# Kernel tuning notes

Measured on AMD Instinct MI355X. Metric: run time of the kernel, lower is better.

The kernel has to match this reference:

```python
import jax, jax.numpy as jnp
import numpy as np

MARGIN = 0.3
N, D = 8192, 128
NUM_CLASSES = 512


def setup_inputs() -> dict:
    key = jax.random.key(0)
    k1, k2 = jax.random.split(key)
    embeddings = jax.random.normal(k1, (N, D), dtype=jnp.float32)
    targets = jax.random.randint(k2, (N,), 0, NUM_CLASSES, dtype=jnp.int64)
    return {"embeddings": embeddings, "targets": targets}


def reference(embeddings, targets):
    x = embeddings.astype(jnp.float32)
    # pairwise squared-euclidean: ||xi||^2 + ||xj||^2 - 2 xi.xj, clamped then sqrt
    sq = jnp.sum(x * x, axis=1)  # [N]
    dist = sq[:, None] + sq[None, :] - 2.0 * (x @ x.T)
    dist = jnp.sqrt(jnp.clip(dist, 1e-12, None))  # [N, N]

    is_pos = targets[:, None] == targets[None, :]  # includes diagonal, as in torch code

    # batch-hard mining: per-row hardest positive (max) and hardest negative (min)
    dist_ap = jnp.max(jnp.where(is_pos, dist, -jnp.inf), axis=1)
    dist_an = jnp.min(jnp.where(is_pos, jnp.inf, dist), axis=1)

    # MarginRankingLoss(margin)(dist_an, dist_ap, y=1) = mean(relu(margin - (dist_an - dist_ap)))
    loss = jnp.mean(jax.nn.relu(dist_ap - dist_an + MARGIN))
    return loss
```

## Files before the change

kernel.cpp:

```cpp
#include <hip/hip_runtime.h>
#include <hip/hip_bf16.h>

#define N_ROWS 8192
#define DIM 128
#define MARGIN_F 0.3f

typedef __attribute__((ext_vector_type(8))) short short8;
typedef __attribute__((ext_vector_type(4))) float f32x4;

__global__ __launch_bounds__(256) void prep_kernel(
    const float* __restrict__ x, const int* __restrict__ tgt,
    unsigned short* __restrict__ xbA, unsigned short* __restrict__ xbB,
    float2* __restrict__ meta, int* __restrict__ apb, int* __restrict__ anb,
    unsigned long long* __restrict__ lsum, unsigned int* __restrict__ lcnt) {
  if (blockIdx.x == 0 && threadIdx.x == 0) { *lsum = 0ull; *lcnt = 0u; }
  const int w = threadIdx.x >> 6, l = threadIdx.x & 63;
  const int row = blockIdx.x * 4 + w;
  float2 v = reinterpret_cast<const float2*>(x + (size_t)row * DIM)[l];
  __hip_bfloat16 b0 = __float2bfloat16(v.x);
  __hip_bfloat16 b1 = __float2bfloat16(v.y);
  __hip_bfloat16 a0 = __float2bfloat16(-2.f * v.x);
  __hip_bfloat16 a1 = __float2bfloat16(-2.f * v.y);
  ushort2 stB, stA;
  stB.x = *reinterpret_cast<unsigned short*>(&b0);
  stB.y = *reinterpret_cast<unsigned short*>(&b1);
  stA.x = *reinterpret_cast<unsigned short*>(&a0);
  stA.y = *reinterpret_cast<unsigned short*>(&a1);
  const int c16 = row >> 4, l15r = row & 15;
  const int unit = c16 * 256 + (l >> 4) * 64 + ((l >> 2) & 3) * 16 + l15r;
  reinterpret_cast<ushort2*>(xbB)[unit * 4 + (l & 3)] = stB;
  reinterpret_cast<ushort2*>(xbA)[unit * 4 + (l & 3)] = stA;

  float s = v.x * v.x + v.y * v.y;
  #pragma unroll
  for (int off = 32; off >= 1; off >>= 1) s += __shfl_xor(s, off);
  if (l == 0) {
    float2 m;
    m.x = s;
    m.y = __int_as_float(tgt[row]);
    meta[row] = m;
    apb[row] = 0x00000000;
    anb[row] = 0x7f800000;
  }
}

__global__ __launch_bounds__(256, 4) void gram_mine_kernel(
    const unsigned short* __restrict__ xbA, const unsigned short* __restrict__ xbB,
    const float2* __restrict__ meta, int* __restrict__ apb, int* __restrict__ anb) {
  const int t = threadIdx.x;
  const int w = t >> 6, l = t & 63;
  const int l15 = l & 15, l4 = l >> 4;
  const int rb = blockIdx.x * 128 + w * 32;
  const int chunk = blockIdx.y * 256;
  const int chunkb = chunk >> 4;

  const short8* xfA = reinterpret_cast<const short8*>(xbA);
  const short8* xfB = reinterpret_cast<const short8*>(xbB);

  short8 a0[4], a1[4];
  #pragma unroll
  for (int kk = 0; kk < 4; ++kk) {
    a0[kk] = xfA[(rb >> 4) * 256 + kk * 64 + l];
    a1[kk] = xfA[((rb >> 4) + 1) * 256 + kk * 64 + l];
  }

  int t_r[8];
  #pragma unroll
  for (int rf = 0; rf < 2; ++rf)
    #pragma unroll
    for (int rg = 0; rg < 4; ++rg)
      t_r[rf * 4 + rg] = __float_as_int(meta[rb + rf * 16 + l4 * 4 + rg].y);

  float ap2[8], an2[8];
  #pragma unroll
  for (int i = 0; i < 8; ++i) { ap2[i] = -__builtin_inff(); an2[i] = __builtin_inff(); }

  #pragma unroll
  for (int ct = 0; ct < 8; ++ct) {
    const int cb16 = chunkb + ct * 2;

    short8 b[8];
    #pragma unroll
    for (int kk = 0; kk < 4; ++kk) {
      b[kk * 2 + 0] = xfB[(cb16 + 0) * 256 + kk * 64 + l];
      b[kk * 2 + 1] = xfB[(cb16 + 1) * 256 + kk * 64 + l];
    }
    float2 mc0 = meta[chunk + ct * 32 + l15];
    float2 mc1 = meta[chunk + ct * 32 + 16 + l15];

    f32x4 acc[2][2];
    {
      f32x4 c0 = {mc0.x, mc0.x, mc0.x, mc0.x};
      f32x4 c1 = {mc1.x, mc1.x, mc1.x, mc1.x};
      acc[0][0] = c0; acc[1][0] = c0;
      acc[0][1] = c1; acc[1][1] = c1;
    }

    __builtin_amdgcn_s_setprio(1);
    #pragma unroll
    for (int kk = 0; kk < 4; ++kk) {
      #pragma unroll
      for (int cf = 0; cf < 2; ++cf) {
        acc[0][cf] = __builtin_amdgcn_mfma_f32_16x16x32_bf16(
            a0[kk], b[kk * 2 + cf], acc[0][cf], 0, 0, 0);
        acc[1][cf] = __builtin_amdgcn_mfma_f32_16x16x32_bf16(
            a1[kk], b[kk * 2 + cf], acc[1][cf], 0, 0, 0);
      }
    }
    __builtin_amdgcn_s_setprio(0);

    #pragma unroll
    for (int cf = 0; cf < 2; ++cf) {
      const int tc = __float_as_int(cf == 0 ? mc0.y : mc1.y);
      #pragma unroll
      for (int rf = 0; rf < 2; ++rf)
        #pragma unroll
        for (int rg = 0; rg < 4; ++rg) {
          const int ix = rf * 4 + rg;
          float v = acc[rf][cf][rg];
          bool p = (t_r[ix] == tc);
          ap2[ix] = p ? fmaxf(ap2[ix], v) : ap2[ix];
          an2[ix] = p ? an2[ix] : fminf(an2[ix], v);
        }
    }
  }

  #pragma unroll
  for (int i = 0; i < 8; ++i) {
    #pragma unroll
    for (int off = 1; off < 16; off <<= 1) {
      ap2[i] = fmaxf(ap2[i], __shfl_xor(ap2[i], off));
      an2[i] = fminf(an2[i], __shfl_xor(an2[i], off));
    }
  }
  if (l15 == 0) {
    #pragma unroll
    for (int rf = 0; rf < 2; ++rf)
      #pragma unroll
      for (int rg = 0; rg < 4; ++rg) {
        int row = rb + rf * 16 + l4 * 4 + rg;
        float sqr = meta[row].x;
        float a2 = fmaxf(ap2[rf * 4 + rg] + sqr, 1e-12f);
        float n2 = fmaxf(an2[rf * 4 + rg] + sqr, 1e-12f);
        atomicMax(apb + row, __float_as_int(a2));
        atomicMin(anb + row, __float_as_int(n2));
      }
  }
}

__global__ __launch_bounds__(1024) void loss_kernel(
    const int* __restrict__ apb, const int* __restrict__ anb,
    unsigned long long* __restrict__ lsum, unsigned int* __restrict__ lcnt,
    float* __restrict__ out) {
  __shared__ float red[16];
  const int i = blockIdx.x * 1024 + threadIdx.x;
  float ap = sqrtf(__int_as_float(apb[i]));
  float an = sqrtf(__int_as_float(anb[i]));
  float li = ap - an + MARGIN_F;
  float s = li > 0.f ? li : 0.f;
  #pragma unroll
  for (int off = 32; off >= 1; off >>= 1) s += __shfl_xor(s, off);
  const int w = threadIdx.x >> 6, l = threadIdx.x & 63;
  if (l == 0) red[w] = s;
  __syncthreads();
  if (threadIdx.x < 16) {
    float v = red[threadIdx.x];
    #pragma unroll
    for (int off = 8; off >= 1; off >>= 1) v += __shfl_xor(v, off);
    if (threadIdx.x == 0) {
      unsigned long long q = (unsigned long long)(long long)((double)v * 4194304.0);
      atomicAdd(lsum, q);
      __threadfence();
      unsigned int old = atomicAdd(lcnt, 1u);
      if (old == gridDim.x - 1) {
        unsigned long long tot = atomicAdd(lsum, 0ull);
        out[0] = (float)((double)tot * (1.0 / 4194304.0) / (double)N_ROWS);
      }
    }
  }
}

extern "C" void kernel_launch(void* const* d_in, const int* in_sizes, int n_in,
                              void* d_out, int out_size, void* d_ws, size_t ws_size,
                              hipStream_t stream) {
  const float* x = (const float*)d_in[0];
  const int* tgt = (const int*)d_in[1];
  float* out = (float*)d_out;

  char* ws = (char*)d_ws;
  unsigned short* xbA = (unsigned short*)ws;
  unsigned short* xbB = (unsigned short*)(ws + 2097152);
  float2* meta = (float2*)(ws + 4194304);
  int* apb = (int*)(ws + 4259840);
  int* anb = (int*)(ws + 4292608);
  unsigned long long* lsum = (unsigned long long*)(ws + 4325376);
  unsigned int* lcnt = (unsigned int*)(ws + 4325384);

  prep_kernel<<<2048, 256, 0, stream>>>(x, tgt, xbA, xbB, meta, apb, anb, lsum, lcnt);
  gram_mine_kernel<<<dim3(64, 32), 256, 0, stream>>>(xbA, xbB, meta, apb, anb);
  loss_kernel<<<8, 1024, 0, stream>>>(apb, anb, lsum, lcnt, out);
}
```

Before: 46.55 us.

## Stage B tiles in swizzled LDS with double-buffered global_load_lds and larger warp tiles

```diff
diff --git a/kernel.cpp b/kernel.cpp
--- a/kernel.cpp
+++ b/kernel.cpp
@@ -8,9 +8,16 @@
 typedef __attribute__((ext_vector_type(8))) short short8;
 typedef __attribute__((ext_vector_type(4))) float f32x4;
 
+typedef const void __attribute__((address_space(1)))* gas1_t;
+typedef void __attribute__((address_space(3)))* las3_t;
+
+__device__ __forceinline__ void load_lds16(const void* g, void* l) {
+  __builtin_amdgcn_global_load_lds((gas1_t)g, (las3_t)l, 16, 0, 0);
+}
+
 __global__ __launch_bounds__(256) void prep_kernel(
     const float* __restrict__ x, const int* __restrict__ tgt,
-    unsigned short* __restrict__ xbA, unsigned short* __restrict__ xbB,
+    unsigned short* __restrict__ xbA, unsigned short* __restrict__ xbBrow,
     float2* __restrict__ meta, int* __restrict__ apb, int* __restrict__ anb,
     unsigned long long* __restrict__ lsum, unsigned int* __restrict__ lcnt) {
   if (blockIdx.x == 0 && threadIdx.x == 0) { *lsum = 0ull; *lcnt = 0u; }
@@ -26,9 +33,9 @@
   stB.y = *reinterpret_cast<unsigned short*>(&b1);
   stA.x = *reinterpret_cast<unsigned short*>(&a0);
   stA.y = *reinterpret_cast<unsigned short*>(&a1);
+  reinterpret_cast<ushort2*>(xbBrow)[(size_t)row * 64 + l] = stB;
   const int c16 = row >> 4, l15r = row & 15;
   const int unit = c16 * 256 + (l >> 4) * 64 + ((l >> 2) & 3) * 16 + l15r;
-  reinterpret_cast<ushort2*>(xbB)[unit * 4 + (l & 3)] = stB;
   reinterpret_cast<ushort2*>(xbA)[unit * 4 + (l & 3)] = stA;
 
   float s = v.x * v.x + v.y * v.y;
@@ -44,76 +51,117 @@
   }
 }
 
-__global__ __launch_bounds__(256, 4) void gram_mine_kernel(
-    const unsigned short* __restrict__ xbA, const unsigned short* __restrict__ xbB,
+__global__ __launch_bounds__(256, 2) void gram_mine_kernel(
+    const unsigned short* __restrict__ xbA, const unsigned short* __restrict__ xbBrow,
     const float2* __restrict__ meta, int* __restrict__ apb, int* __restrict__ anb) {
+  __shared__ unsigned short Bs[2][128 * 128];
+  __shared__ float2 Ms[1024];
+
   const int t = threadIdx.x;
   const int w = t >> 6, l = t & 63;
   const int l15 = l & 15, l4 = l >> 4;
-  const int rb = blockIdx.x * 128 + w * 32;
-  const int chunk = blockIdx.y * 256;
-  const int chunkb = chunk >> 4;
+  const int wr = w >> 1, wc = w & 1;
+  const int rb = blockIdx.x * 128 + wr * 64;
+  const int chunk = blockIdx.y * 1024;
+
+  {
+    #pragma unroll
+    for (int r = 0; r < 2; ++r) {
+      int c = r * 256 + t;
+      load_lds16(reinterpret_cast<const char*>(meta + chunk) + c * 16,
+                 (char*)(&Ms[0]) + c * 16);
+    }
+    #pragma unroll
+    for (int r = 0; r < 8; ++r) {
+      int c = r * 256 + t;
+      int col_local = c >> 4;
+      int off = ((c & 15) * 16) ^ ((col_local & 7) << 4);
+      const char* src = reinterpret_cast<const char*>(xbBrow) +
+                        (size_t)(chunk + col_local) * 256 + off;
+      load_lds16(src, (char*)(&Bs[0][0]) + c * 16);
+    }
+  }
 
   const short8* xfA = reinterpret_cast<const short8*>(xbA);
-  const short8* xfB = reinterpret_cast<const short8*>(xbB);
-
-  short8 a0[4], a1[4];
-  #pragma unroll
-  for (int kk = 0; kk < 4; ++kk) {
-    a0[kk] = xfA[(rb >> 4) * 256 + kk * 64 + l];
-    a1[kk] = xfA[((rb >> 4) + 1) * 256 + kk * 64 + l];
-  }
-
-  int t_r[8];
-  #pragma unroll
-  for (int rf = 0; rf < 2; ++rf)
+
+  short8 a[4][4];
+  #pragma unroll
+  for (int rf = 0; rf < 4; ++rf)
+    #pragma unroll
+    for (int kk = 0; kk < 4; ++kk)
+      a[rf][kk] = xfA[((rb >> 4) + rf) * 256 + kk * 64 + l];
+
+  int t_r[16];
+  #pragma unroll
+  for (int rf = 0; rf < 4; ++rf)
     #pragma unroll
     for (int rg = 0; rg < 4; ++rg)
       t_r[rf * 4 + rg] = __float_as_int(meta[rb + rf * 16 + l4 * 4 + rg].y);
 
-  float ap2[8], an2[8];
-  #pragma unroll
-  for (int i = 0; i < 8; ++i) { ap2[i] = -__builtin_inff(); an2[i] = __builtin_inff(); }
-
-  #pragma unroll
-  for (int ct = 0; ct < 8; ++ct) {
-    const int cb16 = chunkb + ct * 2;
-
-    short8 b[8];
+  float ap2[16], an2[16];
+  #pragma unroll
+  for (int i = 0; i < 16; ++i) { ap2[i] = -__builtin_inff(); an2[i] = __builtin_inff(); }
+
+  #pragma unroll 1
+  for (int s = 0; s < 8; ++s) {
+    if (s < 7) {
+      const int colbase = chunk + (s + 1) * 128;
+      #pragma unroll
+      for (int r = 0; r < 8; ++r) {
+        int c = r * 256 + t;
+        int col_local = c >> 4;
+        int off = ((c & 15) * 16) ^ ((col_local & 7) << 4);
+        const char* src = reinterpret_cast<const char*>(xbBrow) +
+                          (size_t)(colbase + col_local) * 256 + off;
+        load_lds16(src, (char*)(&Bs[(s + 1) & 1][0]) + c * 16);
+      }
+      __builtin_amdgcn_sched_barrier(0);
+      asm volatile("s_waitcnt vmcnt(8)" ::: "memory");
+    } else {
+      __builtin_amdgcn_sched_barrier(0);
+      asm volatile("s_waitcnt vmcnt(0)" ::: "memory");
+    }
+    __builtin_amdgcn_s_barrier();
+    __builtin_amdgcn_sched_barrier(0);
+
+    float2 mc[4];
+    #pragma unroll
+    for (int cf = 0; cf < 4; ++cf)
+      mc[cf] = Ms[s * 128 + wc * 64 + cf * 16 + l15];
+
+    f32x4 acc[4][4];
+    #pragma unroll
+    for (int cf = 0; cf < 4; ++cf) {
+      f32x4 ci = {mc[cf].x, mc[cf].x, mc[cf].x, mc[cf].x};
+      #pragma unroll
+      for (int rf = 0; rf < 4; ++rf) acc[rf][cf] = ci;
+    }
+
+    __builtin_amdgcn_s_setprio(1);
+    const char* bbase = reinterpret_cast<const char*>(&Bs[s & 1][0]);
     #pragma unroll
     for (int kk = 0; kk < 4; ++kk) {
-      b[kk * 2 + 0] = xfB[(cb16 + 0) * 256 + kk * 64 + l];
-      b[kk * 2 + 1] = xfB[(cb16 + 1) * 256 + kk * 64 + l];
-    }
-    float2 mc0 = meta[chunk + ct * 32 + l15];
-    float2 mc1 = meta[chunk + ct * 32 + 16 + l15];
-
-    f32x4 acc[2][2];
-    {
-      f32x4 c0 = {mc0.x, mc0.x, mc0.x, mc0.x};
-      f32x4 c1 = {mc1.x, mc1.x, mc1.x, mc1.x};
-      acc[0][0] = c0; acc[1][0] = c0;
-      acc[0][1] = c1; acc[1][1] = c1;
-    }
-
-    __builtin_amdgcn_s_setprio(1);
-    #pragma unroll
-    for (int kk = 0; kk < 4; ++kk) {
-      #pragma unroll
-      for (int cf = 0; cf < 2; ++cf) {
-        acc[0][cf] = __builtin_amdgcn_mfma_f32_16x16x32_bf16(
-            a0[kk], b[kk * 2 + cf], acc[0][cf], 0, 0, 0);
-        acc[1][cf] = __builtin_amdgcn_mfma_f32_16x16x32_bf16(
-            a1[kk], b[kk * 2 + cf], acc[1][cf], 0, 0, 0);
-      }
+      short8 bfr[4];
+      #pragma unroll
+      for (int cf = 0; cf < 4; ++cf) {
+        int col_local = wc * 64 + cf * 16 + l15;
+        int kb = (kk * 64 + l4 * 16) ^ ((col_local & 7) << 4);
+        bfr[cf] = *reinterpret_cast<const short8*>(bbase + col_local * 256 + kb);
+      }
+      #pragma unroll
+      for (int cf = 0; cf < 4; ++cf)
+        #pragma unroll
+        for (int rf = 0; rf < 4; ++rf)
+          acc[rf][cf] = __builtin_amdgcn_mfma_f32_16x16x32_bf16(
+              a[rf][kk], bfr[cf], acc[rf][cf], 0, 0, 0);
     }
     __builtin_amdgcn_s_setprio(0);
 
     #pragma unroll
-    for (int cf = 0; cf < 2; ++cf) {
-      const int tc = __float_as_int(cf == 0 ? mc0.y : mc1.y);
-      #pragma unroll
-      for (int rf = 0; rf < 2; ++rf)
+    for (int cf = 0; cf < 4; ++cf) {
+      const int tc = __float_as_int(mc[cf].y);
+      #pragma unroll
+      for (int rf = 0; rf < 4; ++rf)
         #pragma unroll
         for (int rg = 0; rg < 4; ++rg) {
           const int ix = rf * 4 + rg;
@@ -123,10 +171,12 @@
           an2[ix] = p ? an2[ix] : fminf(an2[ix], v);
         }
     }
-  }
-
-  #pragma unroll
-  for (int i = 0; i < 8; ++i) {
+
+    if (s < 7) __builtin_amdgcn_s_barrier();
+  }
+
+  #pragma unroll
+  for (int i = 0; i < 16; ++i) {
     #pragma unroll
     for (int off = 1; off < 16; off <<= 1) {
       ap2[i] = fmaxf(ap2[i], __shfl_xor(ap2[i], off));
@@ -135,7 +185,7 @@
   }
   if (l15 == 0) {
     #pragma unroll
-    for (int rf = 0; rf < 2; ++rf)
+    for (int rf = 0; rf < 4; ++rf)
       #pragma unroll
       for (int rg = 0; rg < 4; ++rg) {
         int row = rb + rf * 16 + l4 * 4 + rg;
@@ -189,14 +239,14 @@
 
   char* ws = (char*)d_ws;
   unsigned short* xbA = (unsigned short*)ws;
-  unsigned short* xbB = (unsigned short*)(ws + 2097152);
+  unsigned short* xbBrow = (unsigned short*)(ws + 2097152);
   float2* meta = (float2*)(ws + 4194304);
   int* apb = (int*)(ws + 4259840);
   int* anb = (int*)(ws + 4292608);
   unsigned long long* lsum = (unsigned long long*)(ws + 4325376);
   unsigned int* lcnt = (unsigned int*)(ws + 4325384);
 
-  prep_kernel<<<2048, 256, 0, stream>>>(x, tgt, xbA, xbB, meta, apb, anb, lsum, lcnt);
-  gram_mine_kernel<<<dim3(64, 32), 256, 0, stream>>>(xbA, xbB, meta, apb, anb);
+  prep_kernel<<<2048, 256, 0, stream>>>(x, tgt, xbA, xbBrow, meta, apb, anb, lsum, lcnt);
+  gram_mine_kernel<<<dim3(64, 8), 256, 0, stream>>>(xbA, xbBrow, meta, apb, anb);
   loss_kernel<<<8, 1024, 0, stream>>>(apb, anb, lsum, lcnt, out);
 }
```

After: 51.34 us. +10.3%, slower.
